# Kernel tuning notes

Hardware: AMD Instinct MI355X
Metric: run time of the kernel (lower is better)

## Reference

```python
import jax, jax.numpy as jnp
import numpy as np

B, N_NODES, D = 8, 2048, 256
T = 1024
NUM_MUT = 19  # classes = NUM_MUT + 1 = 20


def setup_inputs() -> dict:
    key = jax.random.key(0)
    k1, k2, k3, k4 = jax.random.split(key, 4)
    gnn_features = jax.random.normal(k1, (B, N_NODES, D), dtype=jnp.float32)
    text_features = jax.random.normal(k2, (B * (NUM_MUT + 1), T, D), dtype=jnp.float32)
    logit_scale = jnp.asarray([100.0], dtype=jnp.float32)  # CLIP-style learned temperature
    seq_to_coords = jax.random.randint(k3, (B, T), 0, N_NODES, dtype=jnp.int64)
    seq_loss_mask = jax.random.uniform(k4, (B, T)) < 0.8
    seq_loss_mask = seq_loss_mask.at[:, 0].set(True)  # guarantee nonzero rows
    return {
        "gnn_features": gnn_features,
        "text_features": text_features,
        "logit_scale": logit_scale,
        "seq_to_coords": seq_to_coords,
        "seq_loss_mask": seq_loss_mask,
    }


def reference(gnn_features, text_features, logit_scale, seq_to_coords, seq_loss_mask):
    # forward_all path of CLIPMutationLoss
    Bb, Nn, Dd = gnn_features.shape
    M1 = text_features.shape[0] // Bb  # num_mutations + 1
    Tt = text_features.shape[1]
    unflattened = text_features.reshape(Bb, M1, Tt, Dd)  # [B, M+1, T, D]
    # gather: selected_gnn[b, t] = gnn_features[b, seq_to_coords[b, t]]
    selected_gnn = jnp.take_along_axis(gnn_features, seq_to_coords[:, :, None], axis=1)  # [B, T, D]
    # per-token dot products across mutation classes
    scores = jnp.einsum("bmtd,btd->bmt", unflattened, selected_gnn) * logit_scale[0]
    # cross-entropy over class dim (axis=1) with target class 0, reduction='none'
    logp = jax.nn.log_softmax(scores, axis=1)
    loss_per_tok = -logp[:, 0, :]  # [B, T]
    mask_f = seq_loss_mask.astype(scores.dtype)
    row_counts = jnp.sum(mask_f, axis=1, keepdims=True)  # loss_weights per row
    loss = jnp.sum(mask_f * loss_per_tok / row_counts) / Bb
    # accuracy over masked tokens
    pred_correct = (jnp.argmax(scores, axis=1) == 0).astype(scores.dtype)  # [B, T]
    acc = jnp.sum(pred_correct * mask_f) / jnp.sum(mask_f)
    return (loss, acc)
```

## Files before the change

kernel.cpp:

```cpp
#include <hip/hip_runtime.h>
#include <hip/hip_bf16.h>

#define B_  8
#define NN  2048
#define D_  256
#define T_  1024
#define M1  20

#define TOK_PER_BLK 16
#define NBLK ((B_ * T_) / TOK_PER_BLK)
#define BLK_PER_B (NBLK / B_)

#define PL 16
#define PC (16 + NBLK)
#define PM (16 + 2 * NBLK)

__global__ __launch_bounds__(1024) void setup_kernel(const uint4* __restrict__ coords_v,
                                                     const uint4* __restrict__ mask_v,
                                                     float* __restrict__ ws)
{
    __shared__ unsigned int s_odd_or;
    __shared__ unsigned int s_gt1_or;
    int tid = threadIdx.x;
    if (tid == 0) { s_odd_or = 0u; s_gt1_or = 0u; }
    __syncthreads();

    unsigned int odd = 0u;
    {
        uint4 a = coords_v[tid];
        uint4 b = coords_v[tid + 1024];
        odd = a.y | a.w | b.y | b.w;
    }
    unsigned int gt = 0u;
    if (tid < 512) {
        uint4 m = mask_v[tid];
        gt = (m.x > 1u) | (m.y > 1u) | (m.z > 1u) | (m.w > 1u);
    }
    if (odd) atomicOr(&s_odd_or, 1u);
    if (gt)  atomicOr(&s_gt1_or, 1u);
    __syncthreads();

    if (tid == 0) ws[0] = (s_odd_or == 0u) ? 1.f : 0.f;
    if (tid == 1) ws[1] = (s_gt1_or != 0u) ? 1.f : 0.f;
}

__device__ __forceinline__ float dot4(float4 a, float4 b) {
    return a.x * b.x + a.y * b.y + a.z * b.z + a.w * b.w;
}

__global__ __launch_bounds__(256) void main_kernel(const float* __restrict__ gnn,
                                                   const float* __restrict__ text,
                                                   const float* __restrict__ scale_p,
                                                   const unsigned int* __restrict__ coords_w,
                                                   const unsigned int* __restrict__ mask_w,
                                                   float* __restrict__ ws)
{
    int tid  = threadIdx.x;
    int lane = tid & 63;
    int wid  = tid >> 6;
    int p    = lane >> 4;
    int q    = lane & 15;
    int token = blockIdx.x * TOK_PER_BLK + wid * 4 + p;
    int b = token >> 10;
    int t = token & (T_ - 1);

    bool coords_i64 = (ws[0] != 0.f);
    bool mask_u8    = (ws[1] != 0.f);

    int idx = coords_i64 ? (int)coords_w[2 * token] : (int)coords_w[token];

    const float4* g4 = (const float4*)(gnn + ((size_t)b * NN + idx) * D_) + 4 * q;
    float4 g0 = g4[0], g1 = g4[1], g2 = g4[2], g3 = g4[3];

    const float4* tb = (const float4*)(text + (((size_t)b * M1) * T_ + t) * D_) + 4 * q;
    float s[M1];
#pragma unroll
    for (int m = 0; m < M1; ++m) {
        const float4* r = tb + (size_t)m * T_ * (D_ / 4);
        float4 t0 = r[0], t1 = r[1], t2 = r[2], t3 = r[3];
        s[m] = dot4(g0, t0) + dot4(g1, t1) + dot4(g2, t2) + dot4(g3, t3);
    }

#pragma unroll
    for (int m = 0; m < M1; ++m) {
        float v = s[m];
        v += __shfl_xor(v, 1, 64);
        v += __shfl_xor(v, 2, 64);
        v += __shfl_xor(v, 4, 64);
        v += __shfl_xor(v, 8, 64);
        s[m] = v;
    }

    float scale = scale_p[0];
    float s0 = s[0] * scale;
    float mx = s0;
#pragma unroll
    for (int m = 1; m < M1; ++m) { s[m] *= scale; mx = fmaxf(mx, s[m]); }
    float sum = __expf(s0 - mx);
#pragma unroll
    for (int m = 1; m < M1; ++m) sum += __expf(s[m] - mx);
    float loss_tok = mx + __logf(sum) - s0;
    float correct  = (s0 >= mx) ? 1.f : 0.f;

    unsigned int mv = mask_u8 ? (unsigned int)((const unsigned char*)mask_w)[token]
                              : mask_w[token];
    float mk = (mv != 0u) ? 1.f : 0.f;

    __shared__ float sl[TOK_PER_BLK], sc[TOK_PER_BLK], sm[TOK_PER_BLK];
    if (q == 0) {
        int slot = wid * 4 + p;
        sl[slot] = mk * loss_tok; sc[slot] = mk * correct; sm[slot] = mk;
    }
    __syncthreads();
    if (tid == 0) {
        float L = 0.f, C = 0.f, M = 0.f;
#pragma unroll
        for (int i = 0; i < TOK_PER_BLK; ++i) { L += sl[i]; C += sc[i]; M += sm[i]; }
        ws[PL + blockIdx.x] = L;
        ws[PC + blockIdx.x] = C;
        ws[PM + blockIdx.x] = M;
    }
}

__global__ __launch_bounds__(512) void finalize_kernel(const float* __restrict__ ws,
                                                       float* __restrict__ out)
{
    int tid  = threadIdx.x;
    int lane = tid & 63;
    int b    = tid >> 6;

    int i = b * BLK_PER_B + lane;
    float l = ws[PL + i];
    float c = ws[PC + i];
    float m = ws[PM + i];
#pragma unroll
    for (int d = 1; d < 64; d <<= 1) {
        l += __shfl_xor(l, d, 64);
        c += __shfl_xor(c, d, 64);
        m += __shfl_xor(m, d, 64);
    }

    __shared__ float sl[B_], sc[B_], sm[B_];
    if (lane == 0) { sl[b] = l / m; sc[b] = c; sm[b] = m; }
    __syncthreads();
    if (tid == 0) {
        float L = 0.f, C = 0.f, M = 0.f;
#pragma unroll
        for (int i2 = 0; i2 < B_; ++i2) { L += sl[i2]; C += sc[i2]; M += sm[i2]; }
        out[0] = L / (float)B_;
        out[1] = C / M;
    }
}

extern "C" void kernel_launch(void* const* d_in, const int* in_sizes, int n_in,
                              void* d_out, int out_size, void* d_ws, size_t ws_size,
                              hipStream_t stream)
{
    const float* gnn           = (const float*)d_in[0];
    const float* text          = (const float*)d_in[1];
    const float* scale         = (const float*)d_in[2];
    const unsigned int* coords = (const unsigned int*)d_in[3];
    const unsigned int* mask   = (const unsigned int*)d_in[4];
    float* ws  = (float*)d_ws;
    float* out = (float*)d_out;

    setup_kernel<<<1, 1024, 0, stream>>>((const uint4*)coords, (const uint4*)mask, ws);
    main_kernel<<<NBLK, 256, 0, stream>>>(gnn, text, scale, coords, mask, ws);
    finalize_kernel<<<1, 512, 0, stream>>>(ws, out);
}
```

Baseline: 38.69 us.

## Split mutation classes across waves, fold dtype detection into main kernel

Each block now handles 4 tokens, with each of its 4 waves computing 5 of the 20 class dot products. Partial scores are exchanged through shared memory, and one wave per token then does the softmax. The separate setup kernel is removed. Each block instead infers the coords and mask dtypes from a small prefix of the inputs, which drops one launch but makes the dtype detection heuristic and weaker. The grid grows fourfold, so the finalize kernel now loops to sum more partials per batch.

Result: slower. 42.67 us (+10.3%).

```diff
diff --git a/kernel.cpp b/kernel.cpp
--- a/kernel.cpp
+++ b/kernel.cpp
@@ -6,8 +6,9 @@
 #define D_  256
 #define T_  1024
 #define M1  20
+#define CPW 5
 
-#define TOK_PER_BLK 16
+#define TOK_PER_BLK 4
 #define NBLK ((B_ * T_) / TOK_PER_BLK)
 #define BLK_PER_B (NBLK / B_)
 
@@ -15,57 +16,45 @@
 #define PC (16 + NBLK)
 #define PM (16 + 2 * NBLK)
 
-__global__ __launch_bounds__(1024) void setup_kernel(const uint4* __restrict__ coords_v,
-                                                     const uint4* __restrict__ mask_v,
-                                                     float* __restrict__ ws)
-{
-    __shared__ unsigned int s_odd_or;
-    __shared__ unsigned int s_gt1_or;
-    int tid = threadIdx.x;
-    if (tid == 0) { s_odd_or = 0u; s_gt1_or = 0u; }
-    __syncthreads();
-
-    unsigned int odd = 0u;
-    {
-        uint4 a = coords_v[tid];
-        uint4 b = coords_v[tid + 1024];
-        odd = a.y | a.w | b.y | b.w;
-    }
-    unsigned int gt = 0u;
-    if (tid < 512) {
-        uint4 m = mask_v[tid];
-        gt = (m.x > 1u) | (m.y > 1u) | (m.z > 1u) | (m.w > 1u);
-    }
-    if (odd) atomicOr(&s_odd_or, 1u);
-    if (gt)  atomicOr(&s_gt1_or, 1u);
-    __syncthreads();
-
-    if (tid == 0) ws[0] = (s_odd_or == 0u) ? 1.f : 0.f;
-    if (tid == 1) ws[1] = (s_gt1_or != 0u) ? 1.f : 0.f;
-}
-
 __device__ __forceinline__ float dot4(float4 a, float4 b) {
     return a.x * b.x + a.y * b.y + a.z * b.z + a.w * b.w;
 }
 
-__global__ __launch_bounds__(256) void main_kernel(const float* __restrict__ gnn,
-                                                   const float* __restrict__ text,
-                                                   const float* __restrict__ scale_p,
-                                                   const unsigned int* __restrict__ coords_w,
-                                                   const unsigned int* __restrict__ mask_w,
-                                                   float* __restrict__ ws)
+__global__ __launch_bounds__(256, 4) void main_kernel(const float* __restrict__ gnn,
+                                                      const float* __restrict__ text,
+                                                      const float* __restrict__ scale_p,
+                                                      const unsigned int* __restrict__ coords_w,
+                                                      const unsigned int* __restrict__ mask_w,
+                                                      float* __restrict__ ws)
 {
     int tid  = threadIdx.x;
     int lane = tid & 63;
-    int wid  = tid >> 6;
+    int w    = tid >> 6;
     int p    = lane >> 4;
     int q    = lane & 15;
-    int token = blockIdx.x * TOK_PER_BLK + wid * 4 + p;
+
+    __shared__ unsigned int s_flags;
+    __shared__ float s_scores[TOK_PER_BLK][M1];
+    __shared__ float s_out[3][TOK_PER_BLK];
+
+    if (tid == 0) s_flags = 0u;
+    __syncthreads();
+    unsigned int det = 0u;
+    if (tid < 16) {
+        uint4 m = ((const uint4*)mask_w)[tid];
+        if ((m.x > 1u) | (m.y > 1u) | (m.z > 1u) | (m.w > 1u)) det = 2u;
+    } else if (tid < 48) {
+        uint4 c = ((const uint4*)coords_w)[tid - 16];
+        if (c.y | c.w) det = 1u;
+    }
+    if (det) atomicOr(&s_flags, det);
+    __syncthreads();
+    bool coords_i64 = !(s_flags & 1u);
+    bool mask_u8    = (s_flags & 2u) != 0u;
+
+    int token = blockIdx.x * TOK_PER_BLK + p;
     int b = token >> 10;
     int t = token & (T_ - 1);
-
-    bool coords_i64 = (ws[0] != 0.f);
-    bool mask_u8    = (ws[1] != 0.f);
 
     int idx = coords_i64 ? (int)coords_w[2 * token] : (int)coords_w[token];
 
@@ -73,49 +62,60 @@
     float4 g0 = g4[0], g1 = g4[1], g2 = g4[2], g3 = g4[3];
 
     const float4* tb = (const float4*)(text + (((size_t)b * M1) * T_ + t) * D_) + 4 * q;
-    float s[M1];
+    float s[CPW];
 #pragma unroll
-    for (int m = 0; m < M1; ++m) {
-        const float4* r = tb + (size_t)m * T_ * (D_ / 4);
+    for (int c = 0; c < CPW; ++c) {
+        const float4* r = tb + (size_t)(w * CPW + c) * T_ * (D_ / 4);
         float4 t0 = r[0], t1 = r[1], t2 = r[2], t3 = r[3];
-        s[m] = dot4(g0, t0) + dot4(g1, t1) + dot4(g2, t2) + dot4(g3, t3);
+        s[c] = dot4(g0, t0) + dot4(g1, t1) + dot4(g2, t2) + dot4(g3, t3);
     }
 
 #pragma unroll
-    for (int m = 0; m < M1; ++m) {
-        float v = s[m];
+    for (int c = 0; c < CPW; ++c) {
+        float v = s[c];
         v += __shfl_xor(v, 1, 64);
         v += __shfl_xor(v, 2, 64);
         v += __shfl_xor(v, 4, 64);
         v += __shfl_xor(v, 8, 64);
-        s[m] = v;
+        s[c] = v;
     }
+    if (q == 0) {
+#pragma unroll
+        for (int c = 0; c < CPW; ++c) s_scores[p][w * CPW + c] = s[c];
+    }
+    __syncthreads();
 
-    float scale = scale_p[0];
-    float s0 = s[0] * scale;
-    float mx = s0;
+    {
+        int tk = blockIdx.x * TOK_PER_BLK + w;
+        float scale = scale_p[0];
+        float sc[M1];
 #pragma unroll
-    for (int m = 1; m < M1; ++m) { s[m] *= scale; mx = fmaxf(mx, s[m]); }
-    float sum = __expf(s0 - mx);
+        for (int m = 0; m < M1; ++m) sc[m] = s_scores[w][m] * scale;
+        float s0 = sc[0];
+        float mx = s0;
 #pragma unroll
-    for (int m = 1; m < M1; ++m) sum += __expf(s[m] - mx);
-    float loss_tok = mx + __logf(sum) - s0;
-    float correct  = (s0 >= mx) ? 1.f : 0.f;
-
-    unsigned int mv = mask_u8 ? (unsigned int)((const unsigned char*)mask_w)[token]
-                              : mask_w[token];
-    float mk = (mv != 0u) ? 1.f : 0.f;
-
-    __shared__ float sl[TOK_PER_BLK], sc[TOK_PER_BLK], sm[TOK_PER_BLK];
-    if (q == 0) {
-        int slot = wid * 4 + p;
-        sl[slot] = mk * loss_tok; sc[slot] = mk * correct; sm[slot] = mk;
+        for (int m = 1; m < M1; ++m) mx = fmaxf(mx, sc[m]);
+        float sum = 0.f;
+#pragma unroll
+        for (int m = 0; m < M1; ++m) sum += __expf(sc[m] - mx);
+        float loss_tok = mx + __logf(sum) - s0;
+        float correct  = (s0 >= mx) ? 1.f : 0.f;
+        unsigned int mv = mask_u8 ? (unsigned int)((const unsigned char*)mask_w)[tk]
+                                  : mask_w[tk];
+        float mk = (mv != 0u) ? 1.f : 0.f;
+        if (lane == 0) {
+            s_out[0][w] = mk * loss_tok;
+            s_out[1][w] = mk * correct;
+            s_out[2][w] = mk;
+        }
     }
     __syncthreads();
     if (tid == 0) {
         float L = 0.f, C = 0.f, M = 0.f;
 #pragma unroll
-        for (int i = 0; i < TOK_PER_BLK; ++i) { L += sl[i]; C += sc[i]; M += sm[i]; }
+        for (int i = 0; i < TOK_PER_BLK; ++i) {
+            L += s_out[0][i]; C += s_out[1][i]; M += s_out[2][i];
+        }
         ws[PL + blockIdx.x] = L;
         ws[PC + blockIdx.x] = C;
         ws[PM + blockIdx.x] = M;
@@ -129,10 +129,14 @@
     int lane = tid & 63;
     int b    = tid >> 6;
 
-    int i = b * BLK_PER_B + lane;
-    float l = ws[PL + i];
-    float c = ws[PC + i];
-    float m = ws[PM + i];
+    float l = 0.f, c = 0.f, m = 0.f;
+#pragma unroll
+    for (int k = 0; k < BLK_PER_B / 64; ++k) {
+        int i = b * BLK_PER_B + k * 64 + lane;
+        l += ws[PL + i];
+        c += ws[PC + i];
+        m += ws[PM + i];
+    }
 #pragma unroll
     for (int d = 1; d < 64; d <<= 1) {
         l += __shfl_xor(l, d, 64);
@@ -140,13 +144,13 @@
         m += __shfl_xor(m, d, 64);
     }
 
-    __shared__ float sl[B_], sc[B_], sm[B_];
-    if (lane == 0) { sl[b] = l / m; sc[b] = c; sm[b] = m; }
+    __shared__ float sl[B_], sc2[B_], sm[B_];
+    if (lane == 0) { sl[b] = l / m; sc2[b] = c; sm[b] = m; }
     __syncthreads();
     if (tid == 0) {
         float L = 0.f, C = 0.f, M = 0.f;
 #pragma unroll
-        for (int i2 = 0; i2 < B_; ++i2) { L += sl[i2]; C += sc[i2]; M += sm[i2]; }
+        for (int i = 0; i < B_; ++i) { L += sl[i]; C += sc2[i]; M += sm[i]; }
         out[0] = L / (float)B_;
         out[1] = C / M;
     }
@@ -164,7 +168,6 @@
     float* ws  = (float*)d_ws;
     float* out = (float*)d_out;
 
-    setup_kernel<<<1, 1024, 0, stream>>>((const uint4*)coords, (const uint4*)mask, ws);
     main_kernel<<<NBLK, 256, 0, stream>>>(gnn, text, scale, coords, mask, ws);
     finalize_kernel<<<1, 512, 0, stream>>>(ws, out);
 }
```
